# Optimization experiments

Hardware: AMD Instinct MI355X
Metric: run time of the kernel (lower is better)

The kernel has to match this reference:

```python
import jax, jax.numpy as jnp
import numpy as np

B, N, C_IN = 4, 2048, 256
H, C_HEAD = 8, 32  # c_out=256, concat=True -> 256//8=32 per head
ALPHA = 0.2
NEG_INF = -9e15

def glorot(key, shape, fan_in, fan_out):
    lim = jnp.sqrt(6.0 / (fan_in + fan_out))
    return jax.random.uniform(key, shape, jnp.float32, -lim, lim)

def setup_inputs() -> dict:
    key = jax.random.key(0)
    k1, k2, k3, k4, k5 = jax.random.split(key, 5)
    x = jax.random.normal(k1, (B, N, C_IN), jnp.float32)
    G = jax.random.randint(k2, (B, N, N), 0, 2, jnp.int32)
    # ensure self-loops so no row is fully masked
    eye = jnp.eye(N, dtype=jnp.int32)[None]
    G = jnp.maximum(G, eye)
    proj_kernel = glorot(k3, (C_IN, H * C_HEAD), C_IN, H * C_HEAD)
    proj_bias = jnp.zeros((H * C_HEAD,), jnp.float32)
    attn_fst = glorot(k4, (H, C_HEAD), H, C_HEAD)
    attn_snd = glorot(k5, (H, C_HEAD), H, C_HEAD)
    return {"x": x, "G": G, "proj_kernel": proj_kernel, "proj_bias": proj_bias,
            "attn_fst": attn_fst, "attn_snd": attn_snd}

def reference(x, G, proj_kernel, proj_bias, attn_fst, attn_snd):
    b, n = x.shape[0], x.shape[1]
    h = (x @ proj_kernel + proj_bias).reshape(b, n, H, C_HEAD)  # [B,N,H,c]
    lf = jnp.einsum('bnhc,hc->bnh', h, attn_fst)  # [B,N,H]
    ls = jnp.einsum('bnhc,hc->bnh', h, attn_snd)  # [B,N,H]
    logit = lf[:, :, None, :] + ls[:, None, :, :]  # [B,N,N,H]
    logit = jax.nn.leaky_relu(logit, negative_slope=ALPHA)
    logit = jnp.where(G[..., None] == 1, logit, NEG_INF)
    attn = jax.nn.softmax(logit, axis=2)
    out = jnp.einsum('bijh,bjhc->bihc', attn, h)  # [B,N,H,c]
    return out.reshape(b, n, H * C_HEAD)  # concat=True
```

## Files before the change

kernel.cpp:

```cpp
#include <hip/hip_runtime.h>

#define BB 4
#define NN 2048
#define CIN 256
#define HH 8
#define COUT 256
#define ALPHAc 0.2f
#define TIP 16
#define TI 8
#define CJ 128

__global__ __launch_bounds__(256) void gat_proj(
    const float* __restrict__ x, const float* __restrict__ W,
    const float* __restrict__ bias, const float* __restrict__ afst,
    const float* __restrict__ asnd, float* __restrict__ hout,
    float* __restrict__ lfout, float* __restrict__ lsout)
{
    const int t = threadIdx.x;
    const int row0 = blockIdx.x * TIP;
    const float* xr = x + (size_t)row0 * CIN;
    const float bv = bias[t];
    float acc[TIP];
#pragma unroll
    for (int r = 0; r < TIP; ++r) acc[r] = bv;
#pragma unroll 2
    for (int k2 = 0; k2 < CIN / 2; ++k2) {
        const float w0 = W[(size_t)(k2 * 2 + 0) * COUT + t];
        const float w1 = W[(size_t)(k2 * 2 + 1) * COUT + t];
#pragma unroll
        for (int r = 0; r < TIP; ++r) {
            const float2 xv = *(const float2*)(xr + r * CIN + k2 * 2);
            acc[r] = fmaf(xv.x, w0, acc[r]);
            acc[r] = fmaf(xv.y, w1, acc[r]);
        }
    }
#pragma unroll
    for (int r = 0; r < TIP; ++r)
        hout[(size_t)(row0 + r) * COUT + t] = acc[r];

    const float af = afst[t], as = asnd[t];
    float f[TIP], s[TIP];
#pragma unroll
    for (int r = 0; r < TIP; ++r) { f[r] = acc[r] * af; s[r] = acc[r] * as; }
#pragma unroll
    for (int off = 16; off; off >>= 1) {
#pragma unroll
        for (int r = 0; r < TIP; ++r) {
            f[r] += __shfl_xor(f[r], off);
            s[r] += __shfl_xor(s[r], off);
        }
    }
    if ((t & 31) == 0) {
        const int hd = t >> 5;
#pragma unroll
        for (int r = 0; r < TIP; ++r) {
            lfout[(size_t)(row0 + r) * HH + hd] = f[r];
            lsout[(size_t)(row0 + r) * HH + hd] = s[r];
        }
    }
}

__device__ __forceinline__ int eoff4(int jl, int h, int half) {
    return jl * 64 + (((h << 3) + (half << 2)) ^ ((jl & 7) << 3));
}

__global__ __launch_bounds__(256) void gat_attn(
    const int* __restrict__ G, const float* __restrict__ hin,
    const float* __restrict__ lf, const float* __restrict__ ls,
    float* __restrict__ out)
{
    __shared__ __align__(16) float e_lds[CJ * 64];
    __shared__ unsigned g_lds[2][CJ];
    __shared__ float lf_lds[TI][HH];
    __shared__ float s_lds[TI][HH];

    const int t = threadIdx.x;
    const int b = blockIdx.x / (NN / TI);
    const int i0 = (blockIdx.x % (NN / TI)) * TI;
    const int h = t >> 5;
    const int jj = t & 31;
    const int w = t >> 6;
    const int l = t & 63;
    const int hh = l >> 3;

    if (t < TI * HH)
        lf_lds[t >> 3][t & 7] = lf[(size_t)(b * NN + i0 + (t >> 3)) * HH + (t & 7)];

    float sp[TI];
    float a[TI][4];
#pragma unroll
    for (int r = 0; r < TI; ++r) {
        sp[r] = 0.f;
#pragma unroll
        for (int c2 = 0; c2 < 4; ++c2) a[r][c2] = 0.f;
    }
    __syncthreads();
    float lfv[TI];
#pragma unroll
    for (int r = 0; r < TI; ++r) lfv[r] = lf_lds[r][h];

    for (int j0 = 0; j0 < NN; j0 += CJ) {
        {
            const int ghalf = t >> 7, col = t & 127;
            const int* gp = G + (size_t)(b * NN + i0 + ghalf * 4) * NN + j0 + col;
            unsigned m = 0;
#pragma unroll
            for (int r = 0; r < 4; ++r)
                m |= (gp[(size_t)r * NN] != 0 ? 1u : 0u) << r;
            g_lds[ghalf][col] = m;
        }
        __syncthreads();
#pragma unroll
        for (int k = 0; k < CJ / 32; ++k) {
            const int jl = jj + 32 * k;
            const float lsv = ls[(size_t)(b * NN + j0 + jl) * HH + h];
            const unsigned gm = g_lds[0][jl] | (g_lds[1][jl] << 4);
            float ev[TI];
#pragma unroll
            for (int r = 0; r < TI; ++r) {
                float xv = lfv[r] + lsv;
                xv = xv > 0.f ? xv : ALPHAc * xv;
                ev[r] = ((gm >> r) & 1u) ? __expf(xv) : 0.f;
                sp[r] += ev[r];
            }
            *(float4*)&e_lds[eoff4(jl, h, 0)] = make_float4(ev[0], ev[1], ev[2], ev[3]);
            *(float4*)&e_lds[eoff4(jl, h, 1)] = make_float4(ev[4], ev[5], ev[6], ev[7]);
        }
        __syncthreads();
#pragma unroll 4
        for (int jl = w; jl < CJ; jl += 4) {
            const float4 hv = *(const float4*)(hin +
                (size_t)(b * NN + j0 + jl) * COUT + (l << 2));
            const float4 lo = *(const float4*)&e_lds[eoff4(jl, hh, 0)];
            const float4 hi = *(const float4*)&e_lds[eoff4(jl, hh, 1)];
            const float ee[8] = {lo.x, lo.y, lo.z, lo.w, hi.x, hi.y, hi.z, hi.w};
            const float hvv[4] = {hv.x, hv.y, hv.z, hv.w};
#pragma unroll
            for (int r = 0; r < TI; ++r)
#pragma unroll
                for (int c2 = 0; c2 < 4; ++c2)
                    a[r][c2] = fmaf(ee[r], hvv[c2], a[r][c2]);
        }
        __syncthreads();
    }
#pragma unroll
    for (int off = 16; off; off >>= 1) {
#pragma unroll
        for (int r = 0; r < TI; ++r) sp[r] += __shfl_xor(sp[r], off);
    }
    if (jj == 0) {
#pragma unroll
        for (int r = 0; r < TI; ++r) s_lds[r][h] = sp[r];
    }
    float* part = e_lds;
#pragma unroll
    for (int r = 0; r < TI; ++r)
#pragma unroll
        for (int c2 = 0; c2 < 4; ++c2)
            part[(w << 11) + ((r * 4 + c2) << 6) + l] = a[r][c2];
    __syncthreads();
#pragma unroll
    for (int kq = 0; kq < 8; ++kq) {
        const int flat = kq * 256 + t;
        const int r = flat >> 8;
        const int c = flat & 255;
        const int rc = ((r * 4 + (c & 3)) << 6) + (c >> 2);
        const float s = part[rc] + part[2048 + rc] + part[4096 + rc] + part[6144 + rc];
        out[(size_t)(b * NN + i0 + r) * COUT + c] = s / s_lds[r][c >> 5];
    }
}

extern "C" void kernel_launch(void* const* d_in, const int* in_sizes, int n_in,
                              void* d_out, int out_size, void* d_ws, size_t ws_size,
                              hipStream_t stream) {
    const float* x    = (const float*)d_in[0];
    const int*   G    = (const int*)d_in[1];
    const float* W    = (const float*)d_in[2];
    const float* bias = (const float*)d_in[3];
    const float* afst = (const float*)d_in[4];
    const float* asnd = (const float*)d_in[5];
    float* out = (float*)d_out;

    float* h_ws  = (float*)d_ws;
    float* lf_ws = h_ws + (size_t)BB * NN * COUT;
    float* ls_ws = lf_ws + (size_t)BB * NN * HH;

    hipLaunchKernelGGL(gat_proj, dim3(BB * NN / TIP), dim3(256), 0, stream,
                       x, W, bias, afst, asnd, h_ws, lf_ws, ls_ws);
    hipLaunchKernelGGL(gat_attn, dim3(BB * (NN / TI)), dim3(256), 0, stream,
                       G, h_ws, lf_ws, ls_ws, out);
}
```

Measured before the change: 333.2 us.

## Tile projection GEMM in LDS, shrink attention chunk, prefetch h, tree-reduce partials

The projection kernel becomes a 128x64 LDS-tiled SGEMM with an 8x4 register tile per thread, and the attention logits are reduced with 8-lane shuffles. The attention kernel halves the j-chunk to 64, which shrinks LDS use and may raise occupancy. It also software-prefetches the next h row, changes the LDS swizzle, and replaces the 4-way partial-sum pass with a pairwise reduction that writes float4 outputs. The gains are better data reuse in the GEMM and lower LDS pressure, paid for with more barriers per j-chunk.

```diff
diff --git a/kernel.cpp b/kernel.cpp
--- a/kernel.cpp
+++ b/kernel.cpp
@@ -6,62 +6,89 @@
 #define HH 8
 #define COUT 256
 #define ALPHAc 0.2f
-#define TIP 16
 #define TI 8
-#define CJ 128
-
+#define CJ 64
+
+#define PBM 128
+#define PBN 64
+#define PKT 16
+#define XLD (PBM + 4)
 __global__ __launch_bounds__(256) void gat_proj(
     const float* __restrict__ x, const float* __restrict__ W,
     const float* __restrict__ bias, const float* __restrict__ afst,
     const float* __restrict__ asnd, float* __restrict__ hout,
     float* __restrict__ lfout, float* __restrict__ lsout)
 {
+    __shared__ float xsT[PKT][XLD];
+    __shared__ float wls[PKT][PBN];
     const int t = threadIdx.x;
-    const int row0 = blockIdx.x * TIP;
-    const float* xr = x + (size_t)row0 * CIN;
-    const float bv = bias[t];
-    float acc[TIP];
-#pragma unroll
-    for (int r = 0; r < TIP; ++r) acc[r] = bv;
-#pragma unroll 2
-    for (int k2 = 0; k2 < CIN / 2; ++k2) {
-        const float w0 = W[(size_t)(k2 * 2 + 0) * COUT + t];
-        const float w1 = W[(size_t)(k2 * 2 + 1) * COUT + t];
-#pragma unroll
-        for (int r = 0; r < TIP; ++r) {
-            const float2 xv = *(const float2*)(xr + r * CIN + k2 * 2);
-            acc[r] = fmaf(xv.x, w0, acc[r]);
-            acc[r] = fmaf(xv.y, w1, acc[r]);
-        }
-    }
-#pragma unroll
-    for (int r = 0; r < TIP; ++r)
-        hout[(size_t)(row0 + r) * COUT + t] = acc[r];
-
-    const float af = afst[t], as = asnd[t];
-    float f[TIP], s[TIP];
-#pragma unroll
-    for (int r = 0; r < TIP; ++r) { f[r] = acc[r] * af; s[r] = acc[r] * as; }
-#pragma unroll
-    for (int off = 16; off; off >>= 1) {
-#pragma unroll
-        for (int r = 0; r < TIP; ++r) {
-            f[r] += __shfl_xor(f[r], off);
-            s[r] += __shfl_xor(s[r], off);
-        }
-    }
-    if ((t & 31) == 0) {
-        const int hd = t >> 5;
-#pragma unroll
-        for (int r = 0; r < TIP; ++r) {
-            lfout[(size_t)(row0 + r) * HH + hd] = f[r];
-            lsout[(size_t)(row0 + r) * HH + hd] = s[r];
+    const int bx = blockIdx.x & 3;
+    const int by = blockIdx.x >> 2;
+    const int row0 = by * PBM, col0 = bx * PBN;
+    const int tx = t & 15, ty = t >> 4;
+
+    float acc[8][4];
+#pragma unroll
+    for (int i = 0; i < 8; ++i)
+#pragma unroll
+        for (int j = 0; j < 4; ++j) acc[i][j] = 0.f;
+
+    for (int kt = 0; kt < CIN; kt += PKT) {
+#pragma unroll
+        for (int s = 0; s < 2; ++s) {
+            const int idx = s * 256 + t;
+            const int row = idx >> 2, kq = (idx & 3) * 4;
+            const float4 v = *(const float4*)(x + (size_t)(row0 + row) * CIN + kt + kq);
+            xsT[kq + 0][row] = v.x; xsT[kq + 1][row] = v.y;
+            xsT[kq + 2][row] = v.z; xsT[kq + 3][row] = v.w;
+        }
+        {
+            const int k = t >> 4, c4 = (t & 15) * 4;
+            *(float4*)&wls[k][c4] = *(const float4*)(W + (size_t)(kt + k) * COUT + col0 + c4);
+        }
+        __syncthreads();
+#pragma unroll
+        for (int k = 0; k < PKT; ++k) {
+            float xv[8], wv[4];
+            *(float4*)&xv[0] = *(const float4*)&xsT[k][ty * 8];
+            *(float4*)&xv[4] = *(const float4*)&xsT[k][ty * 8 + 4];
+            *(float4*)&wv[0] = *(const float4*)&wls[k][tx * 4];
+#pragma unroll
+            for (int i = 0; i < 8; ++i)
+#pragma unroll
+                for (int j = 0; j < 4; ++j)
+                    acc[i][j] = fmaf(xv[i], wv[j], acc[i][j]);
+        }
+        __syncthreads();
+    }
+
+    const float4 bv = *(const float4*)(bias + col0 + tx * 4);
+    const float4 af = *(const float4*)(afst + col0 + tx * 4);
+    const float4 as = *(const float4*)(asnd + col0 + tx * 4);
+    const int hd = (col0 + tx * 4) >> 5;
+#pragma unroll
+    for (int i = 0; i < 8; ++i) {
+        float4 o;
+        o.x = acc[i][0] + bv.x; o.y = acc[i][1] + bv.y;
+        o.z = acc[i][2] + bv.z; o.w = acc[i][3] + bv.w;
+        const int row = row0 + ty * 8 + i;
+        *(float4*)(hout + (size_t)row * COUT + col0 + tx * 4) = o;
+        float pf = o.x * af.x + o.y * af.y + o.z * af.z + o.w * af.w;
+        float ps = o.x * as.x + o.y * as.y + o.z * as.z + o.w * as.w;
+#pragma unroll
+        for (int off = 1; off < 8; off <<= 1) {
+            pf += __shfl_xor(pf, off);
+            ps += __shfl_xor(ps, off);
+        }
+        if ((tx & 7) == 0) {
+            lfout[(size_t)row * HH + hd] = pf;
+            lsout[(size_t)row * HH + hd] = ps;
         }
     }
 }
 
 __device__ __forceinline__ int eoff4(int jl, int h, int half) {
-    return jl * 64 + (((h << 3) + (half << 2)) ^ ((jl & 7) << 3));
+    return jl * 64 + ((((h << 1) + half) ^ (jl & 7)) << 2);
 }
 
 __global__ __launch_bounds__(256) void gat_attn(
@@ -70,7 +97,7 @@
     float* __restrict__ out)
 {
     __shared__ __align__(16) float e_lds[CJ * 64];
-    __shared__ unsigned g_lds[2][CJ];
+    __shared__ unsigned g_lds[4][CJ];
     __shared__ float lf_lds[TI][HH];
     __shared__ float s_lds[TI][HH];
 
@@ -101,20 +128,17 @@
 
     for (int j0 = 0; j0 < NN; j0 += CJ) {
         {
-            const int ghalf = t >> 7, col = t & 127;
-            const int* gp = G + (size_t)(b * NN + i0 + ghalf * 4) * NN + j0 + col;
-            unsigned m = 0;
-#pragma unroll
-            for (int r = 0; r < 4; ++r)
-                m |= (gp[(size_t)r * NN] != 0 ? 1u : 0u) << r;
-            g_lds[ghalf][col] = m;
+            const int col = t & 63;
+            const int* gp = G + (size_t)(b * NN + i0 + 2 * w) * NN + j0 + col;
+            g_lds[w][col] = (gp[0] != 0 ? 1u : 0u) | (gp[NN] != 0 ? 2u : 0u);
         }
         __syncthreads();
 #pragma unroll
         for (int k = 0; k < CJ / 32; ++k) {
             const int jl = jj + 32 * k;
             const float lsv = ls[(size_t)(b * NN + j0 + jl) * HH + h];
-            const unsigned gm = g_lds[0][jl] | (g_lds[1][jl] << 4);
+            const unsigned gm = g_lds[0][jl] | (g_lds[1][jl] << 2) |
+                                (g_lds[2][jl] << 4) | (g_lds[3][jl] << 6);
             float ev[TI];
 #pragma unroll
             for (int r = 0; r < TI; ++r) {
@@ -127,19 +151,25 @@
             *(float4*)&e_lds[eoff4(jl, h, 1)] = make_float4(ev[4], ev[5], ev[6], ev[7]);
         }
         __syncthreads();
-#pragma unroll 4
-        for (int jl = w; jl < CJ; jl += 4) {
-            const float4 hv = *(const float4*)(hin +
-                (size_t)(b * NN + j0 + jl) * COUT + (l << 2));
-            const float4 lo = *(const float4*)&e_lds[eoff4(jl, hh, 0)];
-            const float4 hi = *(const float4*)&e_lds[eoff4(jl, hh, 1)];
-            const float ee[8] = {lo.x, lo.y, lo.z, lo.w, hi.x, hi.y, hi.z, hi.w};
-            const float hvv[4] = {hv.x, hv.y, hv.z, hv.w};
-#pragma unroll
-            for (int r = 0; r < TI; ++r)
-#pragma unroll
-                for (int c2 = 0; c2 < 4; ++c2)
-                    a[r][c2] = fmaf(ee[r], hvv[c2], a[r][c2]);
+        {
+            const float* hbase = hin + (size_t)(b * NN + j0) * COUT + (l << 2);
+            float4 hnext = *(const float4*)(hbase + (size_t)w * COUT);
+#pragma unroll
+            for (int it = 0; it < CJ / 4; ++it) {
+                const int jl = w + it * 4;
+                const float4 hv = hnext;
+                if (it + 1 < CJ / 4)
+                    hnext = *(const float4*)(hbase + (size_t)(jl + 4) * COUT);
+                const float4 lo = *(const float4*)&e_lds[eoff4(jl, hh, 0)];
+                const float4 hi = *(const float4*)&e_lds[eoff4(jl, hh, 1)];
+                const float ee[8] = {lo.x, lo.y, lo.z, lo.w, hi.x, hi.y, hi.z, hi.w};
+                const float hvv[4] = {hv.x, hv.y, hv.z, hv.w};
+#pragma unroll
+                for (int r = 0; r < TI; ++r)
+#pragma unroll
+                    for (int c2 = 0; c2 < 4; ++c2)
+                        a[r][c2] = fmaf(ee[r], hvv[c2], a[r][c2]);
+            }
         }
         __syncthreads();
     }
@@ -152,21 +182,42 @@
 #pragma unroll
         for (int r = 0; r < TI; ++r) s_lds[r][h] = sp[r];
     }
-    float* part = e_lds;
-#pragma unroll
-    for (int r = 0; r < TI; ++r)
-#pragma unroll
-        for (int c2 = 0; c2 < 4; ++c2)
-            part[(w << 11) + ((r * 4 + c2) << 6) + l] = a[r][c2];
-    __syncthreads();
-#pragma unroll
-    for (int kq = 0; kq < 8; ++kq) {
-        const int flat = kq * 256 + t;
-        const int r = flat >> 8;
-        const int c = flat & 255;
-        const int rc = ((r * 4 + (c & 3)) << 6) + (c >> 2);
-        const float s = part[rc] + part[2048 + rc] + part[4096 + rc] + part[6144 + rc];
-        out[(size_t)(b * NN + i0 + r) * COUT + c] = s / s_lds[r][c >> 5];
+    float* buf = e_lds;
+    if (w >= 2) {
+#pragma unroll
+        for (int r = 0; r < TI; ++r)
+#pragma unroll
+            for (int c2 = 0; c2 < 4; ++c2)
+                buf[((w - 2) << 11) + ((r * 4 + c2) << 6) + l] = a[r][c2];
+    }
+    __syncthreads();
+    if (w < 2) {
+#pragma unroll
+        for (int r = 0; r < TI; ++r)
+#pragma unroll
+            for (int c2 = 0; c2 < 4; ++c2)
+                a[r][c2] += buf[(w << 11) + ((r * 4 + c2) << 6) + l];
+    }
+    __syncthreads();
+    if (w == 1) {
+#pragma unroll
+        for (int r = 0; r < TI; ++r)
+#pragma unroll
+            for (int c2 = 0; c2 < 4; ++c2)
+                buf[((r * 4 + c2) << 6) + l] = a[r][c2];
+    }
+    __syncthreads();
+    if (w == 0) {
+#pragma unroll
+        for (int r = 0; r < TI; ++r) {
+            const float inv = 1.f / s_lds[r][hh];
+            float4 o;
+            o.x = (a[r][0] + buf[((r * 4 + 0) << 6) + l]) * inv;
+            o.y = (a[r][1] + buf[((r * 4 + 1) << 6) + l]) * inv;
+            o.z = (a[r][2] + buf[((r * 4 + 2) << 6) + l]) * inv;
+            o.w = (a[r][3] + buf[((r * 4 + 3) << 6) + l]) * inv;
+            *(float4*)(out + (size_t)(b * NN + i0 + r) * COUT + (l << 2)) = o;
+        }
     }
 }
 
@@ -185,8 +236,8 @@
     float* lf_ws = h_ws + (size_t)BB * NN * COUT;
     float* ls_ws = lf_ws + (size_t)BB * NN * HH;
 
-    hipLaunchKernelGGL(gat_proj, dim3(BB * NN / TIP), dim3(256), 0, stream,
-                       x, W, bias, afst, asnd, h_ws, lf_ws, ls_ws);
+    hipLaunchKernelGGL(gat_proj, dim3((BB * NN / PBM) * (COUT / PBN)), dim3(256),
+                       0, stream, x, W, bias, afst, asnd, h_ws, lf_ws, ls_ws);
     hipLaunchKernelGGL(gat_attn, dim3(BB * (NN / TI)), dim3(256), 0, stream,
                        G, h_ws, lf_ws, ls_ws, out);
 }
```

Measured after the change: 326.8 us. Within noise of the previous version (-1.9%).
